# Performance work log

Measured on AMD Instinct MI355X. Metric: run time of the kernel, lower is better.

## Reference

```python
import jax, jax.numpy as jnp
import numpy as np

B, L, D, H = 4, 2048, 1024, 16
HD = D // H  # head_dim = 64


def setup_inputs() -> dict:
    key = jax.random.key(0)
    k1, k2, k3 = jax.random.split(key, 3)
    x = jax.random.normal(k1, (B, L, D), dtype=jnp.float32)
    # causal mask: True where attention is NOT allowed (masked_fill semantics)
    mask = ~jnp.tril(jnp.ones((L, L), dtype=bool))
    Wqkv = jax.random.normal(k2, (3 * D, D), dtype=jnp.float32) * (1.0 / np.sqrt(D))
    bqkv = jnp.zeros((3 * D,), dtype=jnp.float32)
    Wo = jax.random.normal(k3, (D, D), dtype=jnp.float32) * (1.0 / np.sqrt(D))
    bo = jnp.zeros((D,), dtype=jnp.float32)
    return {"x": x, "mask": mask, "Wqkv": Wqkv, "bqkv": bqkv, "Wo": Wo, "bo": bo}


def reference(x, mask, Wqkv, bqkv, Wo, bo):
    b, l, d = x.shape
    qkv = jnp.einsum('bld,ed->ble', x, Wqkv) + bqkv            # [b, l, 3d]
    q, k, v = jnp.split(qkv, 3, axis=-1)
    q = q.reshape(b, l, H, HD).transpose(0, 2, 1, 3)           # [b, h, l, hd]
    k = k.reshape(b, l, H, HD).transpose(0, 2, 1, 3)
    v = v.reshape(b, l, H, HD).transpose(0, 2, 1, 3)
    scale = 1.0 / jnp.sqrt(jnp.float32(HD))
    a = jnp.einsum('bhqd,bhkd->bhqk', q, k) * scale            # [b, h, l, l]
    a = jnp.where(mask, -jnp.inf, a)
    a = jax.nn.softmax(a, axis=-1)
    out = jnp.einsum('bhqk,bhkd->bhqd', a, v)                  # [b, h, l, hd]
    out = out.transpose(0, 2, 1, 3).reshape(b, l, d)
    return jnp.einsum('bld,ed->ble', out, Wo) + bo
```

## Files before the change

### kernel.cpp

```cpp
#include <hip/hip_runtime.h>

typedef __attribute__((ext_vector_type(8))) short short8;
typedef __attribute__((ext_vector_type(4))) float f32x4;
typedef __attribute__((ext_vector_type(16))) float f32x16;
typedef __attribute__((ext_vector_type(2))) int int2v;
typedef __attribute__((ext_vector_type(4))) int int4v;
typedef unsigned short u16;
typedef unsigned int u32;

#define B_ 4
#define L_ 2048
#define D_ 1024
#define H_ 16
#define HD_ 64

__device__ __forceinline__ void load_lds16(const void* g, void* l) {
  __builtin_amdgcn_global_load_lds(
      (__attribute__((address_space(1))) unsigned int*)(g),
      (__attribute__((address_space(3))) unsigned int*)(l),
      16, 0, 0);
}

__device__ __forceinline__ u16 f2bf(float f) {
  union { float f; unsigned u; } c; c.f = f;
  unsigned r = c.u + 0x7FFFu + ((c.u >> 16) & 1u);
  return (u16)(r >> 16);
}

__device__ __forceinline__ u32 cvtpk(float a, float b) {
  u32 r; asm("v_cvt_pk_bf16_f32 %0, %1, %2" : "=v"(r) : "v"(a), "v"(b)); return r;
}

__device__ __forceinline__ int2v trread(u32 addr) {
  int2v r; asm volatile("ds_read_b64_tr_b16 %0, %1" : "=v"(r) : "v"(addr)); return r;
}

__device__ __forceinline__ void pswap(u32& a, u32& b) {
  asm("v_permlane32_swap_b32 %0, %1" : "+v"(a), "+v"(b));
}
__device__ __forceinline__ float xhalf_max(float x) {
  return fmaxf(x, __shfl_xor(x, 32));
}
__device__ __forceinline__ float xhalf_sum(float x) {
  return x + __shfl_xor(x, 32);
}

__global__ __launch_bounds__(256) void cvt_bf16(const float* __restrict__ in,
                                                u16* __restrict__ out, int n) {
  int i = (blockIdx.x * 256 + threadIdx.x) * 4;
  if (i >= n) return;
  float4 v = *(const float4*)(in + i);
  u16 o0 = f2bf(v.x), o1 = f2bf(v.y), o2 = f2bf(v.z), o3 = f2bf(v.w);
  u16* p = out + i;
  p[0] = o0; p[1] = o1; p[2] = o2; p[3] = o3;
}

template <bool BF16_OUT>
__global__ __launch_bounds__(256, 2) void gemm_bt(
    const u16* __restrict__ A, const u16* __restrict__ B,
    const float* __restrict__ bias, void* __restrict__ Cout,
    int M, int N, int K) {
  __shared__ u16 Asm[128 * 32];
  __shared__ u16 Bsm[128 * 32];
  const int tid = threadIdx.x;
  const int lane = tid & 63;
  const int wid = tid >> 6;
  const int fr = lane & 15, fq = lane >> 4;
  const int wr = wid >> 1, wc = wid & 1;
  const long m0 = (long)blockIdx.y * 128;
  const long n0 = (long)blockIdx.x * 128;
  const int srow = lane >> 2;
  const int scol = (lane & 3) * 8;

  f32x4 acc[4][4] = {};

  for (int kt = 0; kt < K; kt += 32) {
    __syncthreads();
#pragma unroll
    for (int c = 0; c < 2; ++c) {
      const int sec = wid * 2 + c;
      load_lds16(A + (m0 + sec * 16 + srow) * K + kt + scol,
                 (char*)Asm + sec * 1024);
      load_lds16(B + (n0 + sec * 16 + srow) * K + kt + scol,
                 (char*)Bsm + sec * 1024);
    }
    __syncthreads();
    short8 af[4], bfr[4];
#pragma unroll
    for (int m = 0; m < 4; ++m)
      af[m] = *(const short8*)((const char*)Asm + (wr * 64 + m * 16 + fr) * 64 + fq * 16);
#pragma unroll
    for (int n = 0; n < 4; ++n)
      bfr[n] = *(const short8*)((const char*)Bsm + (wc * 64 + n * 16 + fr) * 64 + fq * 16);
#pragma unroll
    for (int m = 0; m < 4; ++m)
#pragma unroll
      for (int n = 0; n < 4; ++n)
        acc[m][n] = __builtin_amdgcn_mfma_f32_16x16x32_bf16(af[m], bfr[n], acc[m][n], 0, 0, 0);
  }

  float bv[4];
#pragma unroll
  for (int n = 0; n < 4; ++n) bv[n] = bias[n0 + wc * 64 + n * 16 + fr];

#pragma unroll
  for (int m = 0; m < 4; ++m) {
#pragma unroll
    for (int n = 0; n < 4; ++n) {
      const long col = n0 + wc * 64 + n * 16 + fr;
#pragma unroll
      for (int r = 0; r < 4; ++r) {
        const long row = m0 + wr * 64 + m * 16 + fq * 4 + r;
        float v = acc[m][n][r] + bv[n];
        if (BF16_OUT)
          ((u16*)Cout)[row * N + col] = f2bf(v);
        else
          ((float*)Cout)[row * N + col] = v;
      }
    }
  }
}

__global__ __launch_bounds__(256, 4) void flash_attn6(
    const u16* __restrict__ qkv, u16* __restrict__ attn) {
  __shared__ u16 K2[2][64 * 64];
  __shared__ u16 V2[2][64 * 64];

  const int tid = threadIdx.x;
  const int lane = tid & 63;
  const int wid = tid >> 6;
  const int l31 = lane & 31;
  const int h = lane >> 5;

  const int bh = blockIdx.x;
  const int x = blockIdx.y;
  const long rowbase = (long)(bh >> 4) * L_;
  const int hh = bh & 15;

  const int tbase = (wid < 2) ? (31 - x) * 64 : x * 64;
  const int wq0 = tbase + (wid & 1) * 32;
  const int qg = wq0 + l31;

  short8 qf[4];
  {
    const u16* qp = qkv + (rowbase + qg) * 3072 + hh * 64 + h * 8;
#pragma unroll
    for (int ks = 0; ks < 4; ++ks) qf[ks] = *(const short8*)(qp + ks * 16);
  }

  int krow[2], kvv[2], dvv[2];
#pragma unroll
  for (int c = 0; c < 2; ++c) {
    const int s = (wid * 2 + c) * 8 + (lane >> 3);
    krow[c] = s;
    kvv[c] = ((s >> 2) << 2) + ((lane >> 1) & 3);
    dvv[c] = ((s & 3) << 4) + ((lane & 1) << 3);
  }
  const int kchunk = ((lane & 7) ^ (lane >> 3)) * 8;

  const u32 Vaddr = (u32)(unsigned long long)(__attribute__((address_space(3))) char*)(void*)&V2[0][0];
  const u32 vb0 = Vaddr + ((lane >> 4) & 1) * 128 + (lane & 15) * 8 + h * 1024;

  f32x16 o[2] = {};
  float m_r = -__builtin_inff(), l_r = 0.f;
  const float SC2 = 0.125f * 1.4426950408889634f;

  auto stage = [&](int kt, int buf) {
    const long ktb = (long)kt * 64;
#pragma unroll
    for (int c = 0; c < 2; ++c) {
      load_lds16(qkv + (rowbase + ktb + krow[c]) * 3072 + 1024 + hh * 64 + kchunk,
                 (char*)&K2[buf][0] + (wid * 2 + c) * 1024);
      load_lds16(qkv + (rowbase + ktb + kvv[c]) * 3072 + 2048 + hh * 64 + dvv[c],
                 (char*)&V2[buf][0] + (wid * 2 + c) * 1024);
    }
  };

  const int ktm = 31 - x;
  stage(0, 0);
  __syncthreads();
  int cur = 0;
  for (int kt = 0; kt <= ktm; ++kt) {
    if (kt < ktm) stage(kt + 1, cur ^ 1);
    const int ktb = kt * 64;
    if (ktb <= wq0 + 31) {
      const char* Kb = (const char*)&K2[cur][0];
      const u32 vbB = vb0 + (u32)cur * 8192;

      f32x16 p[2];
      __builtin_amdgcn_s_setprio(1);
#pragma unroll
      for (int t = 0; t < 2; ++t) {
        f32x16 acc = {};
#pragma unroll
        for (int ks = 0; ks < 4; ++ks) {
          const int row = t * 32 + l31;
          short8 kf = *(const short8*)(Kb + row * 128 + (((ks * 2 + h) ^ (row & 7)) * 16));
          acc = __builtin_amdgcn_mfma_f32_32x32x16_bf16(kf, qf[ks], acc, 0, 0, 0);
        }
        p[t] = acc;
      }
      __builtin_amdgcn_s_setprio(0);

      if (ktb + 63 > wq0) {
#pragma unroll
        for (int t = 0; t < 2; ++t)
#pragma unroll
          for (int r = 0; r < 16; ++r) {
            const int kvg = ktb + t * 32 + (r & 3) + 8 * (r >> 2) + 4 * h;
            p[t][r] = (kvg > qg) ? -__builtin_inff() : p[t][r];
          }
      }

      float a[16];
#pragma unroll
      for (int r = 0; r < 16; ++r) a[r] = fmaxf(p[0][r], p[1][r]);
#pragma unroll
      for (int s = 8; s > 0; s >>= 1)
#pragma unroll
        for (int r = 0; r < s; ++r) a[r] = fmaxf(a[r], a[r + s]);
      const float mt = xhalf_max(a[0]);

      if (!__all(mt - m_r <= 44.0f)) {
        const float m_new = fmaxf(m_r, mt);
        const float alpha = __builtin_exp2f((m_r - m_new) * SC2);
#pragma unroll
        for (int t = 0; t < 2; ++t)
#pragma unroll
          for (int r = 0; r < 16; ++r) o[t][r] *= alpha;
        l_r *= alpha;
        m_r = m_new;
      }
      const float msc = m_r * SC2;
#pragma unroll
      for (int t = 0; t < 2; ++t)
#pragma unroll
        for (int r = 0; r < 16; ++r)
          p[t][r] = __builtin_exp2f(fmaf(p[t][r], SC2, -msc));

      float b2[16];
#pragma unroll
      for (int r = 0; r < 16; ++r) b2[r] = p[0][r] + p[1][r];
#pragma unroll
      for (int s = 8; s > 0; s >>= 1)
#pragma unroll
        for (int r = 0; r < s; ++r) b2[r] += b2[r + s];
      l_r += xhalf_sum(b2[0]);

      u32 pf[4][4];
#pragma unroll
      for (int t = 0; t < 2; ++t)
#pragma unroll
        for (int ksl = 0; ksl < 2; ++ksl) {
          u32 x0 = cvtpk(p[t][8 * ksl + 0], p[t][8 * ksl + 1]);
          u32 x1 = cvtpk(p[t][8 * ksl + 2], p[t][8 * ksl + 3]);
          u32 y0 = cvtpk(p[t][8 * ksl + 4], p[t][8 * ksl + 5]);
          u32 y1 = cvtpk(p[t][8 * ksl + 6], p[t][8 * ksl + 7]);
          pswap(x0, y0);
          pswap(x1, y1);
          const int ks = t * 2 + ksl;
          pf[ks][0] = x0; pf[ks][1] = x1; pf[ks][2] = y0; pf[ks][3] = y1;
        }

#pragma unroll
      for (int dt = 0; dt < 2; ++dt) {
        int2v vf[8];
#pragma unroll
        for (int ks = 0; ks < 4; ++ks) {
          vf[ks * 2 + 0] = trread(vbB + dt * 256 + ks * 2048);
          vf[ks * 2 + 1] = trread(vbB + dt * 256 + ks * 2048 + 512);
        }
        asm volatile("s_waitcnt lgkmcnt(0)" ::: "memory");
        __builtin_amdgcn_sched_barrier(0);
        __builtin_amdgcn_s_setprio(1);
#pragma unroll
        for (int ks = 0; ks < 4; ++ks) {
          int4v av;
          av[0] = vf[ks * 2][0]; av[1] = vf[ks * 2][1];
          av[2] = vf[ks * 2 + 1][0]; av[3] = vf[ks * 2 + 1][1];
          int4v pv;
          pv[0] = (int)pf[ks][0]; pv[1] = (int)pf[ks][1];
          pv[2] = (int)pf[ks][2]; pv[3] = (int)pf[ks][3];
          o[dt] = __builtin_amdgcn_mfma_f32_32x32x16_bf16(
              __builtin_bit_cast(short8, av), __builtin_bit_cast(short8, pv),
              o[dt], 0, 0, 0);
        }
        __builtin_amdgcn_s_setprio(0);
      }
    }
    __syncthreads();
    cur ^= 1;
  }

  const float invl = 1.0f / l_r;
  u16* orow = attn + (rowbase + qg) * 1024 + hh * 64;
#pragma unroll
  for (int t = 0; t < 2; ++t)
#pragma unroll
    for (int rp = 0; rp < 8; ++rp) {
      const int r0 = rp * 2;
      const u32 w = cvtpk(o[t][r0] * invl, o[t][r0 + 1] * invl);
      const int d = t * 32 + (r0 & 3) + 8 * (r0 >> 2) + 4 * h;
      *(u32*)(orow + d) = w;
    }
}

extern "C" void kernel_launch(void* const* d_in, const int* in_sizes, int n_in,
                              void* d_out, int out_size, void* d_ws, size_t ws_size,
                              hipStream_t stream) {
  const float* x    = (const float*)d_in[0];
  const float* Wqkv = (const float*)d_in[2];
  const float* bqkv = (const float*)d_in[3];
  const float* Wo   = (const float*)d_in[4];
  const float* bo   = (const float*)d_in[5];
  float* out = (float*)d_out;

  const long ML = (long)B_ * L_;
  u16* xb    = (u16*)d_ws;
  u16* wqkvb = xb + ML * D_;
  u16* wob   = wqkvb + (long)3 * D_ * D_;
  u16* qkv   = wob + (long)D_ * D_;
  u16* attn  = qkv + ML * 3 * D_;

  cvt_bf16<<<dim3((int)(ML * D_ / 1024)), 256, 0, stream>>>(x, xb, (int)(ML * D_));
  cvt_bf16<<<dim3(3 * D_ * D_ / 1024), 256, 0, stream>>>(Wqkv, wqkvb, 3 * D_ * D_);
  cvt_bf16<<<dim3(D_ * D_ / 1024), 256, 0, stream>>>(Wo, wob, D_ * D_);

  gemm_bt<true><<<dim3(3 * D_ / 128, (int)(ML / 128)), 256, 0, stream>>>(
      xb, wqkvb, bqkv, qkv, (int)ML, 3 * D_, D_);

  flash_attn6<<<dim3(64, 16), 256, 0, stream>>>(qkv, attn);

  gemm_bt<false><<<dim3(D_ / 128, (int)(ML / 128)), 256, 0, stream>>>(
      attn, wob, bo, out, (int)ML, D_, D_);
}
```

Measured before the change: 200.5 us.

## Remap GEMM blocks across XCDs and hand-schedule attention LDS reads

The GEMM grid becomes 1D and block IDs are remapped so consecutive tiles land on the same XCD (8-way chiplet interleave), aiming for better L2 reuse. The attention kernel precomputes K LDS addresses, issues explicit ds_read_b128 with a wait after each read, unrolls the V transposed reads using immediate offsets, and lowers launch bounds from 4 to 3 waves. Precomputed addresses add register pressure, and the per-read waitcnt serialises K loads against the MFMAs.

```diff
diff --git a/kernel.cpp b/kernel.cpp
--- a/kernel.cpp
+++ b/kernel.cpp
@@ -31,9 +31,8 @@
   u32 r; asm("v_cvt_pk_bf16_f32 %0, %1, %2" : "=v"(r) : "v"(a), "v"(b)); return r;
 }
 
-__device__ __forceinline__ int2v trread(u32 addr) {
-  int2v r; asm volatile("ds_read_b64_tr_b16 %0, %1" : "=v"(r) : "v"(addr)); return r;
-}
+#define TRREAD(dst, base, OFFLIT) \
+  asm volatile("ds_read_b64_tr_b16 %0, %1 offset:" OFFLIT : "=v"(dst) : "v"(base))
 
 __device__ __forceinline__ void pswap(u32& a, u32& b) {
   asm("v_permlane32_swap_b32 %0, %1" : "+v"(a), "+v"(b));
@@ -67,8 +66,14 @@
   const int wid = tid >> 6;
   const int fr = lane & 15, fq = lane >> 4;
   const int wr = wid >> 1, wc = wid & 1;
-  const long m0 = (long)blockIdx.y * 128;
-  const long n0 = (long)blockIdx.x * 128;
+
+  const int nwg = gridDim.x;
+  const int cpx = nwg >> 3;
+  const int id = (blockIdx.x & 7) * cpx + (blockIdx.x >> 3);
+  const int NBX = N >> 7;
+  const long n0 = (long)(id % NBX) * 128;
+  const long m0 = (long)(id / NBX) * 128;
+
   const int srow = lane >> 2;
   const int scol = (lane & 3) * 8;
 
@@ -121,7 +126,7 @@
   }
 }
 
-__global__ __launch_bounds__(256, 4) void flash_attn6(
+__global__ __launch_bounds__(256, 3) void flash_attn7(
     const u16* __restrict__ qkv, u16* __restrict__ attn) {
   __shared__ u16 K2[2][64 * 64];
   __shared__ u16 V2[2][64 * 64];
@@ -158,7 +163,16 @@
   }
   const int kchunk = ((lane & 7) ^ (lane >> 3)) * 8;
 
+  const u32 Kaddr = (u32)(unsigned long long)(__attribute__((address_space(3))) char*)(void*)&K2[0][0];
   const u32 Vaddr = (u32)(unsigned long long)(__attribute__((address_space(3))) char*)(void*)&V2[0][0];
+  u32 koff[2][4];
+#pragma unroll
+  for (int t = 0; t < 2; ++t) {
+    const int row = t * 32 + l31;
+#pragma unroll
+    for (int ks = 0; ks < 4; ++ks)
+      koff[t][ks] = Kaddr + (u32)(row * 128 + (((ks * 2 + h) ^ (row & 7)) * 16));
+  }
   const u32 vb0 = Vaddr + ((lane >> 4) & 1) * 128 + (lane & 15) * 8 + h * 1024;
 
   f32x16 o[2] = {};
@@ -184,8 +198,7 @@
     if (kt < ktm) stage(kt + 1, cur ^ 1);
     const int ktb = kt * 64;
     if (ktb <= wq0 + 31) {
-      const char* Kb = (const char*)&K2[cur][0];
-      const u32 vbB = vb0 + (u32)cur * 8192;
+      const u32 curoff = (u32)cur * 8192;
 
       f32x16 p[2];
       __builtin_amdgcn_s_setprio(1);
@@ -194,8 +207,9 @@
         f32x16 acc = {};
 #pragma unroll
         for (int ks = 0; ks < 4; ++ks) {
-          const int row = t * 32 + l31;
-          short8 kf = *(const short8*)(Kb + row * 128 + (((ks * 2 + h) ^ (row & 7)) * 16));
+          short8 kf;
+          asm volatile("ds_read_b128 %0, %1" : "=v"(kf) : "v"(koff[t][ks] + curoff));
+          asm volatile("s_waitcnt lgkmcnt(0)" ::: "memory");
           acc = __builtin_amdgcn_mfma_f32_32x32x16_bf16(kf, qf[ks], acc, 0, 0, 0);
         }
         p[t] = acc;
@@ -262,31 +276,48 @@
           pf[ks][0] = x0; pf[ks][1] = x1; pf[ks][2] = y0; pf[ks][3] = y1;
         }
 
-#pragma unroll
-      for (int dt = 0; dt < 2; ++dt) {
-        int2v vf[8];
-#pragma unroll
-        for (int ks = 0; ks < 4; ++ks) {
-          vf[ks * 2 + 0] = trread(vbB + dt * 256 + ks * 2048);
-          vf[ks * 2 + 1] = trread(vbB + dt * 256 + ks * 2048 + 512);
-        }
-        asm volatile("s_waitcnt lgkmcnt(0)" ::: "memory");
-        __builtin_amdgcn_sched_barrier(0);
-        __builtin_amdgcn_s_setprio(1);
-#pragma unroll
-        for (int ks = 0; ks < 4; ++ks) {
-          int4v av;
-          av[0] = vf[ks * 2][0]; av[1] = vf[ks * 2][1];
-          av[2] = vf[ks * 2 + 1][0]; av[3] = vf[ks * 2 + 1][1];
-          int4v pv;
-          pv[0] = (int)pf[ks][0]; pv[1] = (int)pf[ks][1];
-          pv[2] = (int)pf[ks][2]; pv[3] = (int)pf[ks][3];
-          o[dt] = __builtin_amdgcn_mfma_f32_32x32x16_bf16(
-              __builtin_bit_cast(short8, av), __builtin_bit_cast(short8, pv),
-              o[dt], 0, 0, 0);
-        }
-        __builtin_amdgcn_s_setprio(0);
-      }
+      const u32 vbB = vb0 + curoff;
+      int2v vf[8];
+      TRREAD(vf[0], vbB, "0");    TRREAD(vf[1], vbB, "512");
+      TRREAD(vf[2], vbB, "2048"); TRREAD(vf[3], vbB, "2560");
+      TRREAD(vf[4], vbB, "4096"); TRREAD(vf[5], vbB, "4608");
+      TRREAD(vf[6], vbB, "6144"); TRREAD(vf[7], vbB, "6656");
+      asm volatile("s_waitcnt lgkmcnt(0)" ::: "memory");
+      __builtin_amdgcn_sched_barrier(0);
+      __builtin_amdgcn_s_setprio(1);
+#pragma unroll
+      for (int ks = 0; ks < 4; ++ks) {
+        int4v av;
+        av[0] = vf[ks * 2][0]; av[1] = vf[ks * 2][1];
+        av[2] = vf[ks * 2 + 1][0]; av[3] = vf[ks * 2 + 1][1];
+        int4v pv;
+        pv[0] = (int)pf[ks][0]; pv[1] = (int)pf[ks][1];
+        pv[2] = (int)pf[ks][2]; pv[3] = (int)pf[ks][3];
+        o[0] = __builtin_amdgcn_mfma_f32_32x32x16_bf16(
+            __builtin_bit_cast(short8, av), __builtin_bit_cast(short8, pv),
+            o[0], 0, 0, 0);
+      }
+      __builtin_amdgcn_s_setprio(0);
+      TRREAD(vf[0], vbB, "256");  TRREAD(vf[1], vbB, "768");
+      TRREAD(vf[2], vbB, "2304"); TRREAD(vf[3], vbB, "2816");
+      TRREAD(vf[4], vbB, "4352"); TRREAD(vf[5], vbB, "4864");
+      TRREAD(vf[6], vbB, "6400"); TRREAD(vf[7], vbB, "6912");
+      asm volatile("s_waitcnt lgkmcnt(0)" ::: "memory");
+      __builtin_amdgcn_sched_barrier(0);
+      __builtin_amdgcn_s_setprio(1);
+#pragma unroll
+      for (int ks = 0; ks < 4; ++ks) {
+        int4v av;
+        av[0] = vf[ks * 2][0]; av[1] = vf[ks * 2][1];
+        av[2] = vf[ks * 2 + 1][0]; av[3] = vf[ks * 2 + 1][1];
+        int4v pv;
+        pv[0] = (int)pf[ks][0]; pv[1] = (int)pf[ks][1];
+        pv[2] = (int)pf[ks][2]; pv[3] = (int)pf[ks][3];
+        o[1] = __builtin_amdgcn_mfma_f32_32x32x16_bf16(
+            __builtin_bit_cast(short8, av), __builtin_bit_cast(short8, pv),
+            o[1], 0, 0, 0);
+      }
+      __builtin_amdgcn_s_setprio(0);
     }
     __syncthreads();
     cur ^= 1;
@@ -326,11 +357,11 @@
   cvt_bf16<<<dim3(3 * D_ * D_ / 1024), 256, 0, stream>>>(Wqkv, wqkvb, 3 * D_ * D_);
   cvt_bf16<<<dim3(D_ * D_ / 1024), 256, 0, stream>>>(Wo, wob, D_ * D_);
 
-  gemm_bt<true><<<dim3(3 * D_ / 128, (int)(ML / 128)), 256, 0, stream>>>(
+  gemm_bt<true><<<dim3((3 * D_ / 128) * (int)(ML / 128)), 256, 0, stream>>>(
       xb, wqkvb, bqkv, qkv, (int)ML, 3 * D_, D_);
 
-  flash_attn6<<<dim3(64, 16), 256, 0, stream>>>(qkv, attn);
-
-  gemm_bt<false><<<dim3(D_ / 128, (int)(ML / 128)), 256, 0, stream>>>(
+  flash_attn7<<<dim3(64, 16), 256, 0, stream>>>(qkv, attn);
+
+  gemm_bt<false><<<dim3((D_ / 128) * (int)(ML / 128)), 256, 0, stream>>>(
       attn, wob, bo, out, (int)ML, D_, D_);
 }
```

New measurement: 199.8 us. No clear change (-0.3%).
